# Optimization experiments

Hardware: AMD Instinct MI355X
Metric: run time of the kernel (lower is better)

Reference implementation:

```python
import jax, jax.numpy as jnp
import numpy as np

TEMP = 0.05  # contrastive temperature (ContrastiveLoss.temp)
N, D = 8192, 128


def setup_inputs() -> dict:
    key = jax.random.key(0)
    k1, k2 = jax.random.split(key)
    x = jax.random.normal(k1, (N, D), dtype=jnp.float32)
    # Binary positive-pair label matrix; diagonal forced to 1 so every row
    # has at least one positive (positive_pair_nums > 0).
    y = (jax.random.uniform(k2, (N, N)) < 0.05).astype(jnp.float32)
    y = jnp.maximum(y, jnp.eye(N, dtype=jnp.float32))
    return {"x": x, "y": y}


def reference(x, y):
    # similarity(): L2-normalize rows, cosine matmul, exp(cos / temp)
    x_norm = x / jnp.linalg.norm(x, axis=1, keepdims=True)        # [N, D]
    cos_sim = jnp.exp(jnp.matmul(x_norm, x_norm.T) / TEMP)        # [N, N]

    positive_pair_nums = jnp.sum(y, axis=-1)                      # [N]
    neg_y = 1.0 - y
    # hard_mode == 'normal': negative mass per anchor
    nl = jnp.sum(cos_sim * neg_y, axis=-1, keepdims=True)         # [N, 1]

    # sm = log(cos_sim / (cos_sim + nl)); average over positives per row
    sm = jnp.log(cos_sim / (cos_sim + nl))                        # [N, N]
    lm = jnp.sum(sm * y, axis=-1) / positive_pair_nums            # [N]
    return -jnp.mean(lm)
```

## Files before the change

### kernel.cpp

```cpp
#include <hip/hip_runtime.h>
#include <hip/hip_bf16.h>


#define NN 8192

typedef short bf16x8 __attribute__((ext_vector_type(8)));
typedef float f32x4 __attribute__((ext_vector_type(4)));
typedef unsigned long long u64;
typedef unsigned int u32;

__device__ inline unsigned short f32_to_bf16_rne(float f) {
    unsigned u = __float_as_uint(f);
    unsigned r = 0x7FFFu + ((u >> 16) & 1u);
    return (unsigned short)((u + r) >> 16);
}

__global__ __launch_bounds__(256) void prep_kernel(
    const float* __restrict__ x, const float* __restrict__ y,
    unsigned short* __restrict__ xn, u64* __restrict__ bits) {
    const int t = threadIdx.x;
    const int w = t >> 6, l = t & 63;
    if (blockIdx.x < 2048) {
        const int row = blockIdx.x * 4 + w;
        float2 v = reinterpret_cast<const float2*>(x)[row * 64 + l];
        float ss = v.x * v.x + v.y * v.y;
#pragma unroll
        for (int m = 1; m < 64; m <<= 1) ss += __shfl_xor(ss, m);
        float rn = 1.0f / sqrtf(ss);
        ushort2 st;
        st.x = f32_to_bf16_rne(v.x * rn);
        st.y = f32_to_bf16_rne(v.y * rn);
        reinterpret_cast<ushort2*>(xn)[row * 64 + l] = st;
    } else {
        const int r = (blockIdx.x - 2048) * 4 + w;
        const float4* yr =
            reinterpret_cast<const float4*>(y + (size_t)r * NN);
        u64* br = bits + (size_t)r * 128;
#pragma unroll 4
        for (int g = 0; g < 32; ++g) {
            float4 v = yr[g * 64 + l];
            u64 m0 = __ballot(v.x != 0.0f);
            u64 m1 = __ballot(v.y != 0.0f);
            u64 m2 = __ballot(v.z != 0.0f);
            u64 m3 = __ballot(v.w != 0.0f);
            if (l == 0) {
                br[g * 4 + 0] = m0;
                br[g * 4 + 1] = m1;
                br[g * 4 + 2] = m2;
                br[g * 4 + 3] = m3;
            }
        }
    }
}

template <bool DIAG>
__device__ __forceinline__ void epilogue(
    const f32x4 (&acc)[4][2], const u32 (&W0)[4], const u32 (&W1)[4],
    int shbase, int wM, int wN, int lm16, int lh, int l, int rb, int cb,
    float* __restrict__ PtT, float* __restrict__ PtA, float* __restrict__ PtY,
    float* __restrict__ sdg) {
#pragma unroll
    for (int qq = 0; qq < 2; ++qq) {
        float T = 0.0f, A = 0.0f, Y = 0.0f;
        const int rl = wN * 32 + qq * 16 + lm16;
#pragma unroll
        for (int p = 0; p < 4; ++p) {
            const int cl = wM * 64 + p * 16 + lh * 4;
#pragma unroll
            for (int j = 0; j < 4; ++j) {
                float s = 20.0f * acc[p][qq][j];
                float e = __expf(s);
                u32 word = qq ? W1[j] : W0[j];
                u32 bit = (word >> (shbase + p * 4)) & 1u;
                if (DIAG) {
                    if (cl + j == rl) {
                        sdg[rb * 128 + rl] = s;
                        e = 0.0f;
                        bit = 0u;
                    }
                }
                T += e;
                A += bit ? s : 0.0f;
                Y += bit ? e : 0.0f;
            }
        }
        T += __shfl_xor(T, 16); T += __shfl_xor(T, 32);
        A += __shfl_xor(A, 16); A += __shfl_xor(A, 32);
        Y += __shfl_xor(Y, 16); Y += __shfl_xor(Y, 32);
        if (l < 16) {
            const size_t idx =
                (size_t)(rb * 128 + wN * 32 + qq * 16 + l) * 128 + cb * 2 + wM;
            PtT[idx] = T;
            PtA[idx] = A;
            PtY[idx] = Y;
        }
    }
}

__global__ __launch_bounds__(512, 4) void contrast_main_kernel(
    const unsigned short* __restrict__ xn, const u64* __restrict__ bits,
    float* __restrict__ PtT, float* __restrict__ PtA, float* __restrict__ PtY,
    float* __restrict__ sdg) {
    __shared__ __align__(1024) char lds[65536];

    const int bid = blockIdx.x;
    const int swz = (bid & 7) * 512 + (bid >> 3);
    const int cb = swz & 63, rb = swz >> 6;
    const int t = threadIdx.x;
    const int w = t >> 6, l = t & 63;
    const int wM = w & 1, wN = w >> 1;
    const int lm16 = l & 15, lh = l >> 4;

    const int g4 = (cb >> 1) * 4;
    const int rbase = rb * 128 + wN * 32;
    u64 B0[4], B1[4];
    {
        const u64* bp0 = bits + (size_t)(rbase + lm16) * 128 + g4;
        const u64* bp1 = bits + (size_t)(rbase + 16 + lm16) * 128 + g4;
        ulonglong2 a0 = *reinterpret_cast<const ulonglong2*>(bp0);
        ulonglong2 a1 = *reinterpret_cast<const ulonglong2*>(bp0 + 2);
        ulonglong2 c0 = *reinterpret_cast<const ulonglong2*>(bp1);
        ulonglong2 c1 = *reinterpret_cast<const ulonglong2*>(bp1 + 2);
        B0[0] = a0.x; B0[1] = a0.y; B0[2] = a1.x; B0[3] = a1.y;
        B1[0] = c0.x; B1[1] = c0.y; B1[2] = c1.x; B1[3] = c1.y;
    }
    const int base = (cb & 1) * 32 + wM * 16;
    const bool hi = base >= 32;
    u32 W0[4], W1[4];
#pragma unroll
    for (int e = 0; e < 4; ++e) {
        W0[e] = hi ? (u32)(B0[e] >> 32) : (u32)B0[e];
        W1[e] = hi ? (u32)(B1[e] >> 32) : (u32)B1[e];
    }
    const int shbase = (base & 31) + lh;

    {
        const char* xb = reinterpret_cast<const char*>(xn);
        const char* srcA = xb + (size_t)cb * 32768;
        const char* srcB = xb + (size_t)rb * 32768;
#pragma unroll
        for (int i = 0; i < 8; ++i) {
            const int p = i * 8192 + t * 16;
            const int pp = p & 32767;
            const int src = pp ^ (((pp >> 8) & 7) << 4);
            __builtin_amdgcn_global_load_lds(
                (const __attribute__((address_space(1))) void*)(
                    (i < 4 ? srcA : srcB) + src),
                (__attribute__((address_space(3))) void*)(lds + p), 16, 0, 0);
        }
    }
    asm volatile("s_waitcnt vmcnt(0)" ::: "memory");
    __syncthreads();

    f32x4 acc[4][2];
#pragma unroll
    for (int i = 0; i < 4; ++i)
#pragma unroll
        for (int j = 0; j < 2; ++j) {
            f32x4 z = {0.0f, 0.0f, 0.0f, 0.0f};
            acc[i][j] = z;
        }

#pragma unroll
    for (int ks = 0; ks < 4; ++ks) {
        bf16x8 af[4], bfr[2];
#pragma unroll
        for (int p = 0; p < 4; ++p) {
            const int c = wM * 64 + p * 16 + lm16;
            const int v = c * 256 + ks * 64 + lh * 16;
            af[p] = *reinterpret_cast<const bf16x8*>(lds + (v ^ ((c & 7) << 4)));
        }
#pragma unroll
        for (int qq = 0; qq < 2; ++qq) {
            const int r = wN * 32 + qq * 16 + lm16;
            const int v = r * 256 + ks * 64 + lh * 16;
            bfr[qq] = *reinterpret_cast<const bf16x8*>(
                lds + 32768 + (v ^ ((r & 7) << 4)));
        }
#pragma unroll
        for (int p = 0; p < 4; ++p)
#pragma unroll
            for (int qq = 0; qq < 2; ++qq)
                acc[p][qq] = __builtin_amdgcn_mfma_f32_16x16x32_bf16(
                    af[p], bfr[qq], acc[p][qq], 0, 0, 0);
    }

    if (rb == cb)
        epilogue<true>(acc, W0, W1, shbase, wM, wN, lm16, lh, l, rb, cb, PtT,
                       PtA, PtY, sdg);
    else
        epilogue<false>(acc, W0, W1, shbase, wM, wN, lm16, lh, l, rb, cb, PtT,
                        PtA, PtY, sdg);
}

__global__ __launch_bounds__(1024) void finalize_kernel(
    const float* __restrict__ PtT, const float* __restrict__ PtA,
    const float* __restrict__ PtY, const u64* __restrict__ bits,
    const float* __restrict__ sdg, float* __restrict__ rowloss) {
    const int t = threadIdx.x;
    const int w = t >> 6, l = t & 63;
    const int r = blockIdx.x * 16 + w;

    float2 vT = reinterpret_cast<const float2*>(PtT + (size_t)r * 128)[l];
    float2 vA = reinterpret_cast<const float2*>(PtA + (size_t)r * 128)[l];
    float2 vY = reinterpret_cast<const float2*>(PtY + (size_t)r * 128)[l];
    ulonglong2 bb =
        reinterpret_cast<const ulonglong2*>(bits + (size_t)r * 128)[l];
    float T = vT.x + vT.y, A = vA.x + vA.y, Y = vY.x + vY.y;
    float P = (float)(__popcll(bb.x) + __popcll(bb.y));
#pragma unroll
    for (int m = 1; m < 64; m <<= 1) {
        T += __shfl_xor(T, m);
        A += __shfl_xor(A, m);
        Y += __shfl_xor(Y, m);
        P += __shfl_xor(P, m);
    }
    if (l == 0) {
        const float nl = T - Y;
        rowloss[r] =
            (A - (P - 1.0f) * logf(nl) - log1pf(nl * __expf(-sdg[r]))) / P;
    }
}

__global__ void reduce_kernel(const float* __restrict__ rowloss,
                              float* __restrict__ out) {
    __shared__ float red[256];
    const int t = threadIdx.x;
    float s = 0.0f;
#pragma unroll
    for (int i = 0; i < 8; ++i) {
        float4 v = reinterpret_cast<const float4*>(rowloss)[i * 256 + t];
        s += v.x + v.y + v.z + v.w;
    }
    red[t] = s;
    __syncthreads();
    for (int k = 128; k > 0; k >>= 1) {
        if (t < k) red[t] += red[t + k];
        __syncthreads();
    }
    if (t == 0) out[0] = -red[0] / (float)NN;
}

extern "C" void kernel_launch(void* const* d_in, const int* in_sizes, int n_in,
                              void* d_out, int out_size, void* d_ws,
                              size_t ws_size, hipStream_t stream) {
    const float* x = (const float*)d_in[0];
    const float* y = (const float*)d_in[1];

    char* ws = (char*)d_ws;
    unsigned short* xn = (unsigned short*)ws;
    u64* bits = (u64*)(ws + (2ull << 20));
    float* PtT = (float*)(ws + (10ull << 20));
    float* PtA = (float*)(ws + (14ull << 20));
    float* PtY = (float*)(ws + (18ull << 20));
    float* sdg = (float*)(ws + (22ull << 20));
    float* rowloss = (float*)(ws + (22ull << 20) + 32768);

    prep_kernel<<<4096, 256, 0, stream>>>(x, y, xn, bits);
    contrast_main_kernel<<<4096, 512, 0, stream>>>(xn, bits, PtT, PtA, PtY,
                                                   sdg);
    finalize_kernel<<<512, 1024, 0, stream>>>(PtT, PtA, PtY, bits, sdg,
                                              rowloss);
    reduce_kernel<<<1, 256, 0, stream>>>(rowloss, (float*)d_out);
}
```

Before: 411.4 us.

## Pre-reduce partials in LDS and fuse finalize with the final reduction

The main kernel now combines its two column-half partial sums per row through a small LDS buffer. It writes one T/A/Y value per row and column block in a column-major layout, which halves the partial-sum traffic and makes the finalize reads coalesced. Each row's positive count is taken with popcount during the bit-packing pass in prep. The diagonal term uses the constant exp(-1/temp) rather than the stored diagonal logit. Finalize and reduce are merged into one kernel that uses a block reduction and an atomicAdd after a memset, in exchange for an extra __syncthreads in the main kernel and a nondeterministic atomic summation order.

```diff
diff --git a/kernel.cpp b/kernel.cpp
--- a/kernel.cpp
+++ b/kernel.cpp
@@ -17,7 +17,8 @@
 
 __global__ __launch_bounds__(256) void prep_kernel(
     const float* __restrict__ x, const float* __restrict__ y,
-    unsigned short* __restrict__ xn, u64* __restrict__ bits) {
+    unsigned short* __restrict__ xn, u64* __restrict__ bits,
+    float* __restrict__ Pp) {
     const int t = threadIdx.x;
     const int w = t >> 6, l = t & 63;
     if (blockIdx.x < 2048) {
@@ -36,6 +37,7 @@
         const float4* yr =
             reinterpret_cast<const float4*>(y + (size_t)r * NN);
         u64* br = bits + (size_t)r * 128;
+        int pc = 0;
 #pragma unroll 4
         for (int g = 0; g < 32; ++g) {
             float4 v = yr[g * 64 + l];
@@ -43,6 +45,7 @@
             u64 m1 = __ballot(v.y != 0.0f);
             u64 m2 = __ballot(v.z != 0.0f);
             u64 m3 = __ballot(v.w != 0.0f);
+            pc += __popcll(m0) + __popcll(m1) + __popcll(m2) + __popcll(m3);
             if (l == 0) {
                 br[g * 4 + 0] = m0;
                 br[g * 4 + 1] = m1;
@@ -50,15 +53,15 @@
                 br[g * 4 + 3] = m3;
             }
         }
+        if (l == 0) Pp[r] = (float)pc;
     }
 }
 
 template <bool DIAG>
 __device__ __forceinline__ void epilogue(
     const f32x4 (&acc)[4][2], const u32 (&W0)[4], const u32 (&W1)[4],
-    int shbase, int wM, int wN, int lm16, int lh, int l, int rb, int cb,
-    float* __restrict__ PtT, float* __restrict__ PtA, float* __restrict__ PtY,
-    float* __restrict__ sdg) {
+    int shbase, int wM, int wN, int lm16, int lh, int l,
+    float* __restrict__ Lb) {
 #pragma unroll
     for (int qq = 0; qq < 2; ++qq) {
         float T = 0.0f, A = 0.0f, Y = 0.0f;
@@ -74,7 +77,6 @@
                 u32 bit = (word >> (shbase + p * 4)) & 1u;
                 if (DIAG) {
                     if (cl + j == rl) {
-                        sdg[rb * 128 + rl] = s;
                         e = 0.0f;
                         bit = 0u;
                     }
@@ -88,20 +90,20 @@
         A += __shfl_xor(A, 16); A += __shfl_xor(A, 32);
         Y += __shfl_xor(Y, 16); Y += __shfl_xor(Y, 32);
         if (l < 16) {
-            const size_t idx =
-                (size_t)(rb * 128 + wN * 32 + qq * 16 + l) * 128 + cb * 2 + wM;
-            PtT[idx] = T;
-            PtA[idx] = A;
-            PtY[idx] = Y;
+            const int r = wN * 32 + qq * 16 + l;
+            Lb[(wM * 3 + 0) * 128 + r] = T;
+            Lb[(wM * 3 + 1) * 128 + r] = A;
+            Lb[(wM * 3 + 2) * 128 + r] = Y;
         }
     }
 }
 
 __global__ __launch_bounds__(512, 4) void contrast_main_kernel(
     const unsigned short* __restrict__ xn, const u64* __restrict__ bits,
-    float* __restrict__ PtT, float* __restrict__ PtA, float* __restrict__ PtY,
-    float* __restrict__ sdg) {
-    __shared__ __align__(1024) char lds[65536];
+    float* __restrict__ PtT, float* __restrict__ PtA,
+    float* __restrict__ PtY) {
+    __shared__ __align__(1024) char lds[68608];
+    float* Lb = reinterpret_cast<float*>(lds + 65536);
 
     const int bid = blockIdx.x;
     const int swz = (bid & 7) * 512 + (bid >> 3);
@@ -186,59 +188,45 @@
     }
 
     if (rb == cb)
-        epilogue<true>(acc, W0, W1, shbase, wM, wN, lm16, lh, l, rb, cb, PtT,
-                       PtA, PtY, sdg);
+        epilogue<true>(acc, W0, W1, shbase, wM, wN, lm16, lh, l, Lb);
     else
-        epilogue<false>(acc, W0, W1, shbase, wM, wN, lm16, lh, l, rb, cb, PtT,
-                        PtA, PtY, sdg);
-}
-
-__global__ __launch_bounds__(1024) void finalize_kernel(
+        epilogue<false>(acc, W0, W1, shbase, wM, wN, lm16, lh, l, Lb);
+    __syncthreads();
+
+    if (t < 128) {
+        const size_t o = (size_t)cb * NN + rb * 128 + t;
+        PtT[o] = Lb[0 * 128 + t] + Lb[3 * 128 + t];
+        PtA[o] = Lb[1 * 128 + t] + Lb[4 * 128 + t];
+        PtY[o] = Lb[2 * 128 + t] + Lb[5 * 128 + t];
+    }
+}
+
+__global__ __launch_bounds__(256) void finalize_kernel(
     const float* __restrict__ PtT, const float* __restrict__ PtA,
-    const float* __restrict__ PtY, const u64* __restrict__ bits,
-    const float* __restrict__ sdg, float* __restrict__ rowloss) {
+    const float* __restrict__ PtY, const float* __restrict__ Pp,
+    float* __restrict__ out) {
     const int t = threadIdx.x;
-    const int w = t >> 6, l = t & 63;
-    const int r = blockIdx.x * 16 + w;
-
-    float2 vT = reinterpret_cast<const float2*>(PtT + (size_t)r * 128)[l];
-    float2 vA = reinterpret_cast<const float2*>(PtA + (size_t)r * 128)[l];
-    float2 vY = reinterpret_cast<const float2*>(PtY + (size_t)r * 128)[l];
-    ulonglong2 bb =
-        reinterpret_cast<const ulonglong2*>(bits + (size_t)r * 128)[l];
-    float T = vT.x + vT.y, A = vA.x + vA.y, Y = vY.x + vY.y;
-    float P = (float)(__popcll(bb.x) + __popcll(bb.y));
-#pragma unroll
-    for (int m = 1; m < 64; m <<= 1) {
-        T += __shfl_xor(T, m);
-        A += __shfl_xor(A, m);
-        Y += __shfl_xor(Y, m);
-        P += __shfl_xor(P, m);
-    }
-    if (l == 0) {
-        const float nl = T - Y;
-        rowloss[r] =
-            (A - (P - 1.0f) * logf(nl) - log1pf(nl * __expf(-sdg[r]))) / P;
-    }
-}
-
-__global__ void reduce_kernel(const float* __restrict__ rowloss,
-                              float* __restrict__ out) {
+    const int r = blockIdx.x * 256 + t;
+    float T = 0.0f, A = 0.0f, Y = 0.0f;
+#pragma unroll 8
+    for (int cb = 0; cb < 64; ++cb) {
+        T += PtT[(size_t)cb * NN + r];
+        A += PtA[(size_t)cb * NN + r];
+        Y += PtY[(size_t)cb * NN + r];
+    }
+    const float P = Pp[r];
+    const float nl = T - Y;
+    const float lm =
+        (A - (P - 1.0f) * logf(nl) - log1pf(nl * 2.0611536e-9f)) / P;
+
     __shared__ float red[256];
-    const int t = threadIdx.x;
-    float s = 0.0f;
-#pragma unroll
-    for (int i = 0; i < 8; ++i) {
-        float4 v = reinterpret_cast<const float4*>(rowloss)[i * 256 + t];
-        s += v.x + v.y + v.z + v.w;
-    }
-    red[t] = s;
+    red[t] = lm;
     __syncthreads();
     for (int k = 128; k > 0; k >>= 1) {
         if (t < k) red[t] += red[t + k];
         __syncthreads();
     }
-    if (t == 0) out[0] = -red[0] / (float)NN;
+    if (t == 0) atomicAdd(out, -red[0] * (1.0f / (float)NN));
 }
 
 extern "C" void kernel_launch(void* const* d_in, const int* in_sizes, int n_in,
@@ -251,15 +239,13 @@
     unsigned short* xn = (unsigned short*)ws;
     u64* bits = (u64*)(ws + (2ull << 20));
     float* PtT = (float*)(ws + (10ull << 20));
-    float* PtA = (float*)(ws + (14ull << 20));
-    float* PtY = (float*)(ws + (18ull << 20));
-    float* sdg = (float*)(ws + (22ull << 20));
-    float* rowloss = (float*)(ws + (22ull << 20) + 32768);
-
-    prep_kernel<<<4096, 256, 0, stream>>>(x, y, xn, bits);
-    contrast_main_kernel<<<4096, 512, 0, stream>>>(xn, bits, PtT, PtA, PtY,
-                                                   sdg);
-    finalize_kernel<<<512, 1024, 0, stream>>>(PtT, PtA, PtY, bits, sdg,
-                                              rowloss);
-    reduce_kernel<<<1, 256, 0, stream>>>(rowloss, (float*)d_out);
-}
+    float* PtA = (float*)(ws + (12ull << 20));
+    float* PtY = (float*)(ws + (14ull << 20));
+    float* Pp = (float*)(ws + (16ull << 20));
+
+    hipMemsetAsync(d_out, 0, sizeof(float), stream);
+    prep_kernel<<<4096, 256, 0, stream>>>(x, y, xn, bits, Pp);
+    contrast_main_kernel<<<4096, 512, 0, stream>>>(xn, bits, PtT, PtA, PtY);
+    finalize_kernel<<<NN / 256, 256, 0, stream>>>(PtT, PtA, PtY, Pp,
+                                                  (float*)d_out);
+}
```

After: 410.9 us. Within noise of the previous version (-0.1%).
